# Kernel optimization log

Hardware: AMD Instinct MI355X
Metric: run time of the kernel (lower is better)

## Reference

```python
import jax, jax.numpy as jnp
import numpy as np


def conv2d(x, w, b, stride, pad):
    y = jax.lax.conv_general_dilated(
        x, w, (stride, stride), [(pad, pad), (pad, pad)],
        dimension_numbers=('NCHW', 'OIHW', 'NCHW'))
    return y + b[None, :, None, None]


def setup_inputs() -> dict:
    key = jax.random.key(0)
    ks = jax.random.split(key, 12)
    B = 8
    s = 0.02
    return {
        'x1': jax.random.normal(ks[0], (B, 256, 128, 128), jnp.float32),
        'x2': jax.random.normal(ks[1], (B, 512, 64, 64), jnp.float32),
        'x3': jax.random.normal(ks[2], (B, 1024, 32, 32), jnp.float32),
        'x4': jax.random.normal(ks[3], (B, 2048, 16, 16), jnp.float32),
        'cov1_w': jax.random.normal(ks[4], (512, 256, 3, 3), jnp.float32) * s,
        'cov1_b': jnp.zeros((512,), jnp.float32),
        'cov2_w': jax.random.normal(ks[5], (512, 512, 3, 3), jnp.float32) * s,
        'cov2_b': jnp.zeros((512,), jnp.float32),
        'cov3_w': jax.random.normal(ks[6], (512, 1024, 3, 3), jnp.float32) * s,
        'cov3_b': jnp.zeros((512,), jnp.float32),
        'cov4_w': jax.random.normal(ks[7], (512, 2048, 1, 1), jnp.float32) * s,
        'cov4_b': jnp.zeros((512,), jnp.float32),
        'gce_fc1_w': jax.random.normal(ks[8], (8, 64, 256), jnp.float32) * s,
        'gce_fc1_b': jnp.zeros((8, 64), jnp.float32),
        'gce_fc2_w': jax.random.normal(ks[9], (8, 256, 64), jnp.float32) * s,
        'gce_fc2_b': jnp.zeros((8, 256), jnp.float32),
        'gce_sa_w': jax.random.normal(ks[10], (8, 256), jnp.float32) * s,
        'gce_sa_b': jnp.zeros((8,), jnp.float32),
    }


def reference(x1, x2, x3, x4,
              cov1_w, cov1_b, cov2_w, cov2_b, cov3_w, cov3_b, cov4_w, cov4_b,
              gce_fc1_w, gce_fc1_b, gce_fc2_w, gce_fc2_b, gce_sa_w, gce_sa_b):
    # NOTE (faithful to original): DSCA.forward overwrites its attention output
    # with `rearrange(x, 'b (h w) c -> b c h w')`, i.e. it returns its first
    # argument (cov4(x4)) unchanged. Hence cov1/cov2/cov3 and the whole
    # dynamic-top-k attention path are dead code with exactly-zero gradients;
    # omitting them yields identical outputs and identical (zero) grads.
    x4 = conv2d(x4, cov4_w, cov4_b, 1, 0)          # [B,512,16,16]
    x = jnp.concatenate([x4, x4, x4, x4], axis=1)  # [B,2048,16,16]
    x0 = x
    B, C, H, W = x.shape
    G = 8
    xg = x.reshape(B, G, C // G, H, W)             # [B,G,256,H,W]
    # ChannelAttention per group (reduction_ratio=4: 256->64->256)
    avg = xg.mean(axis=(3, 4))                                           # [B,G,256]
    h = jax.nn.relu(jnp.einsum('bgc,goc->bgo', avg, gce_fc1_w) + gce_fc1_b)
    ca = jax.nn.sigmoid(jnp.einsum('bgo,gco->bgc', h, gce_fc2_w) + gce_fc2_b)
    y = xg * ca[:, :, :, None, None]
    # SpatialAttention per group (1x1 conv to 1 channel)
    sa = jax.nn.sigmoid(jnp.einsum('bgchw,gc->bghw', y, gce_sa_w)
                        + gce_sa_b[None, :, None, None])
    y = y * sa[:, :, None, :, :]
    # GroupCBAMEnhancer gating: sigmoid, then hard-1 above per-group mean
    y = jax.nn.sigmoid(y)
    mean = y.mean(axis=(2, 3, 4), keepdims=True)   # mean over (c,h,w) per group
    mask = jnp.where(y > mean, jnp.float32(1.0), y).reshape(B, C, H, W)
    return x * mask + x0
```

## Files before the change

### kernel.cpp

```cpp
#include <hip/hip_runtime.h>
#include <math.h>

typedef __attribute__((ext_vector_type(8))) short bf16x8;
typedef __attribute__((ext_vector_type(8))) unsigned short u16x8;
typedef __attribute__((ext_vector_type(4))) float f32x4;

#define GLOAD_LDS16(g, l) __builtin_amdgcn_global_load_lds( \
    (const __attribute__((address_space(1))) unsigned int*)(g), \
    (__attribute__((address_space(3))) unsigned int*)(l), 16, 0, 0)

__device__ __forceinline__ unsigned short f2bf(float f) {
    unsigned int u = __builtin_bit_cast(unsigned int, f);
    unsigned int r = (u + 0x7FFFu + ((u >> 16) & 1)) >> 16;
    return (unsigned short)r;
}

__device__ __forceinline__ float sigmoidf_(float v) {
    return 1.f / (1.f + expf(-v));
}

__global__ __launch_bounds__(256) void convert_kernel(
    const float* __restrict__ w, const float* __restrict__ x4,
    unsigned short* __restrict__ wbf, unsigned short* __restrict__ xbf)
{
    __shared__ float t[64][65];
    if (blockIdx.x < 512) {
        int f = blockIdx.x * 256 + threadIdx.x;
        int tile = f >> 9, inner = f & 511;
        int r = inner >> 3, cc = inner & 7;
        int mt = tile >> 5, kt = tile & 31;
        const float* src = w + (mt * 64 + r) * 2048 + kt * 64 + cc * 8;
        float4 v0 = *(const float4*)src;
        float4 v1 = *(const float4*)(src + 4);
        u16x8 o;
        o[0] = f2bf(v0.x); o[1] = f2bf(v0.y); o[2] = f2bf(v0.z); o[3] = f2bf(v0.w);
        o[4] = f2bf(v1.x); o[5] = f2bf(v1.y); o[6] = f2bf(v1.z); o[7] = f2bf(v1.w);
        *(u16x8*)(wbf + (size_t)tile * 4096 + r * 64 + ((cc ^ (r & 7)) * 8)) = o;
        return;
    }
    const int bi = blockIdx.x - 512;
    const int b = bi >> 7, rem = bi & 127;
    const int kt = rem >> 2, pg = rem & 3;
    const float* src = x4 + ((size_t)b * 2048 + kt * 64) * 256 + pg * 64;
#pragma unroll
    for (int i = 0; i < 4; ++i) {
        int f = i * 256 + threadIdx.x;
        int kk = f >> 4, pp4 = f & 15;
        float4 v = *(const float4*)(src + kk * 256 + pp4 * 4);
        t[pp4 * 4 + 0][kk] = v.x;
        t[pp4 * 4 + 1][kk] = v.y;
        t[pp4 * 4 + 2][kk] = v.z;
        t[pp4 * 4 + 3][kk] = v.w;
    }
    __syncthreads();
    unsigned short* dst = xbf + (size_t)((b * 4 + pg) * 32 + kt) * 4096;
#pragma unroll
    for (int i = 0; i < 2; ++i) {
        int inner = i * 256 + threadIdx.x;
        int r = inner >> 3, cc = inner & 7;
        u16x8 o;
#pragma unroll
        for (int j = 0; j < 8; ++j) o[j] = f2bf(t[r][cc * 8 + j]);
        *(u16x8*)(dst + r * 64 + ((cc ^ (r & 7)) * 8)) = o;
    }
}

__global__ __launch_bounds__(256) void gemm_bf16(
    const unsigned short* __restrict__ wbf, const unsigned short* __restrict__ xbf,
    const float* __restrict__ bias, float* __restrict__ y4,
    float* __restrict__ chanpart)
{
    __shared__ short As[2][2048];
    __shared__ short Bs[2][4096];

    const int tid = threadIdx.x;
    const int wave = tid >> 6, lane = tid & 63;
    const int wm = wave >> 1, wn = wave & 1;
    const int lr = lane & 15, lh = lane >> 4;

    const int nt = blockIdx.x;
    const int mt = blockIdx.y;

    const unsigned short* Abase = wbf + ((size_t)(mt >> 1) * 32) * 4096 + (mt & 1) * 2048;
    const unsigned short* Bbase = xbf + (size_t)nt * 32 * 4096;

#define STAGE(buf, t)                                                         \
    {                                                                         \
        const unsigned short* A_ = Abase + (size_t)(t) * 4096;                \
        const unsigned short* B_ = Bbase + (size_t)(t) * 4096;                \
        _Pragma("unroll")                                                     \
        for (int q2 = 0; q2 < 3; ++q2) {                                      \
            int seg = wave * 3 + q2;                                          \
            if (seg < 4) {                                                    \
                GLOAD_LDS16(A_ + seg * 512 + lane * 8, &As[buf][seg * 512]);  \
            } else {                                                          \
                GLOAD_LDS16(B_ + (seg - 4) * 512 + lane * 8,                  \
                            &Bs[buf][(seg - 4) * 512]);                       \
            }                                                                 \
        }                                                                     \
    }

    STAGE(0, 0);
    __syncthreads();

    f32x4 acc[2] = {};
    int cur = 0;
    for (int t = 0; t < 32; ++t) {
        if (t < 31) STAGE(cur ^ 1, t + 1);
#pragma unroll
        for (int kc = 0; kc < 2; ++kc) {
            const int ch = kc * 4 + lh;
            int rA  = wm * 16 + lr;
            int rB0 = wn * 32 + lr, rB1 = rB0 + 16;
            bf16x8 a0 = *(const bf16x8*)(&As[cur][rA  * 64 + ((ch ^ (rA  & 7)) * 8)]);
            bf16x8 b0 = *(const bf16x8*)(&Bs[cur][rB0 * 64 + ((ch ^ (rB0 & 7)) * 8)]);
            bf16x8 b1 = *(const bf16x8*)(&Bs[cur][rB1 * 64 + ((ch ^ (rB1 & 7)) * 8)]);
            acc[0] = __builtin_amdgcn_mfma_f32_16x16x32_bf16(a0, b0, acc[0], 0, 0, 0);
            acc[1] = __builtin_amdgcn_mfma_f32_16x16x32_bf16(a0, b1, acc[1], 0, 0, 0);
        }
        __syncthreads();
        cur ^= 1;
    }
#undef STAGE

    const int b = nt >> 2, q = nt & 3;
    float* yb = y4 + ((size_t)b * 512 + mt * 32) * 256 + q * 64;
#pragma unroll
    for (int rr = 0; rr < 4; ++rr) {
        const int m = wm * 16 + lh * 4 + rr;
        const float bv = bias[mt * 32 + m];
        yb[m * 256 + wn * 32 + lr]      = acc[0][rr] + bv;
        yb[m * 256 + wn * 32 + 16 + lr] = acc[1][rr] + bv;
        float s = acc[0][rr] + acc[1][rr];
        s += __shfl_xor(s, 1);
        s += __shfl_xor(s, 2);
        s += __shfl_xor(s, 4);
        s += __shfl_xor(s, 8);
        if (lr == 0)
            chanpart[(size_t)(b * 512 + mt * 32 + m) * 8 + q * 2 + wn] = s + 32.f * bv;
    }
}

__global__ __launch_bounds__(256) void sa_kernel(
    const float* __restrict__ y4, const float* __restrict__ chanpart,
    const float* __restrict__ fc1w, const float* __restrict__ fc1b,
    const float* __restrict__ fc2w, const float* __restrict__ fc2b,
    const float* __restrict__ saw, const float* __restrict__ sab,
    float* __restrict__ ca, float* __restrict__ sa, float* __restrict__ gsums)
{
    const int blk = blockIdx.x;
    const int bg = blk >> 3, pc = blk & 7;
    const int b = bg >> 3, g = bg & 7;
    const int tid = threadIdx.x;
    const float* xg = y4 + ((size_t)b * 512 + (g & 1) * 256) * 256;

    __shared__ float avgs[256], red[256], hs[64], cas[256], caws[256], sas[32];

    {
        const float* cpp = chanpart + (size_t)(b * 512 + (g & 1) * 256 + tid) * 8;
        float cp = 0.f;
#pragma unroll
        for (int i = 0; i < 8; ++i) cp += cpp[i];
        avgs[tid] = cp * (1.f / 256.f);
    }
    __syncthreads();
    {
        int o = tid & 63, seg = tid >> 6;
        const float* wr = fc1w + (g * 64 + o) * 256 + seg * 64;
        const float* av = avgs + seg * 64;
        float s = 0.f;
#pragma unroll
        for (int i = 0; i < 64; ++i) s = fmaf(av[i], wr[i], s);
        red[tid] = s;
    }
    __syncthreads();
    if (tid < 64) {
        float s = fc1b[g * 64 + tid] + red[tid] + red[64 + tid] + red[128 + tid] + red[192 + tid];
        hs[tid] = fmaxf(s, 0.f);
    }
    __syncthreads();
    {
        const float* wr = fc2w + (g * 256 + tid) * 64;
        float s = fc2b[g * 256 + tid];
#pragma unroll
        for (int i = 0; i < 64; ++i) s = fmaf(hs[i], wr[i], s);
        float v = sigmoidf_(s);
        cas[tid] = v;
        caws[tid] = v * saw[g * 256 + tid];
        if (pc == 0) ca[bg * 256 + tid] = v;
    }
    __syncthreads();
    const int p_l = tid & 31, seg8 = tid >> 5;
    const int p = pc * 32 + p_l;
    {
        float s = 0.f;
#pragma unroll
        for (int i = 0; i < 32; ++i) {
            int c = seg8 * 32 + i;
            s = fmaf(xg[c * 256 + p], caws[c], s);
        }
        red[tid] = s;
    }
    __syncthreads();
    if (tid < 32) {
        float s = sab[g];
#pragma unroll
        for (int k = 0; k < 8; ++k) s += red[k * 32 + tid];
        float v = sigmoidf_(s);
        sas[tid] = v;
        sa[bg * 256 + pc * 32 + tid] = v;
    }
    __syncthreads();
    {
        float sv = sas[p_l];
        float s = 0.f;
#pragma unroll
        for (int i = 0; i < 32; ++i) {
            int c = seg8 * 32 + i;
            s += sigmoidf_(xg[c * 256 + p] * cas[c] * sv);
        }
        red[tid] = s;
    }
    __syncthreads();
    for (int off = 128; off > 0; off >>= 1) {
        if (tid < off) red[tid] += red[tid + off];
        __syncthreads();
    }
    if (tid == 0) gsums[blk] = red[0];
}

__global__ __launch_bounds__(256) void final_kernel(
    const float* __restrict__ y4, const float* __restrict__ ca,
    const float* __restrict__ sa, const float* __restrict__ gsums,
    float* __restrict__ out)
{
    int f = blockIdx.x * 256 + threadIdx.x;
    int p4 = f & 63, ch = (f >> 6) & 2047, b = f >> 17;
    int g = ch >> 8, c = ch & 255, bg = b * 8 + g;
    const float4 x = *(const float4*)(y4 + ((size_t)b * 512 + (g & 1) * 256 + c) * 256 + p4 * 4);
    float cav = ca[bg * 256 + c];
    const float4 sv = *(const float4*)(sa + bg * 256 + p4 * 4);
    float msum = 0.f;
#pragma unroll
    for (int i = 0; i < 8; ++i) msum += gsums[bg * 8 + i];
    float mean = msum * (1.f / 65536.f);
    float4 o;
#define DOLANE(X) { float yv = sigmoidf_(x.X * cav * sv.X); float mk = (yv > mean) ? 1.f : yv; o.X = x.X * (1.f + mk); }
    DOLANE(x) DOLANE(y) DOLANE(z) DOLANE(w)
#undef DOLANE
    *(float4*)(out + (size_t)f * 4) = o;
}

extern "C" void kernel_launch(void* const* d_in, const int* in_sizes, int n_in,
                              void* d_out, int out_size, void* d_ws, size_t ws_size,
                              hipStream_t stream) {
    const float* x4   = (const float*)d_in[3];
    const float* w4   = (const float*)d_in[10];
    const float* b4   = (const float*)d_in[11];
    const float* fc1w = (const float*)d_in[12];
    const float* fc1b = (const float*)d_in[13];
    const float* fc2w = (const float*)d_in[14];
    const float* fc2b = (const float*)d_in[15];
    const float* saw  = (const float*)d_in[16];
    const float* sab  = (const float*)d_in[17];
    float* out = (float*)d_out;

    float* ws = (float*)d_ws;
    float* y4       = ws;
    float* ca       = ws + 1048576;
    float* sa       = ws + 1064960;
    float* gsums    = ws + 1081344;
    float* chanpart = ws + 1081856;
    unsigned short* wbf = (unsigned short*)(ws + 1114624);
    unsigned short* xbf = (unsigned short*)(ws + 1638912);

    convert_kernel<<<dim3(1536), dim3(256), 0, stream>>>(w4, x4, wbf, xbf);
    gemm_bf16<<<dim3(32, 16), dim3(256), 0, stream>>>(wbf, xbf, b4, y4, chanpart);
    sa_kernel<<<dim3(512), dim3(256), 0, stream>>>(y4, chanpart, fc1w, fc1b, fc2w, fc2b,
                                                   saw, sab, ca, sa, gsums);
    final_kernel<<<dim3(4096), dim3(256), 0, stream>>>(y4, ca, sa, gsums, out);
}
```

Baseline: 52.49 us.

## Halve GEMM N-tile to 1024 blocks with XCD-aware mapping; stage y4 slice in LDS

The GEMM N tile shrinks from 64 to 32 columns, doubling the grid to 1024 blocks so more CUs get work. Each wave now issues one MFMA per k-chunk, and the per-channel partial sums grow to 16 slots per channel. Block indices are remapped so consecutive XCDs share N tiles, aiming for better L2 reuse. The spatial-attention kernel now loads its 256x32 y4 slice into LDS once and reuses it for both channel passes, replacing two strided global reads. The cost is less compute per loaded tile in the GEMM and a 32 KB LDS footprint in sa_kernel.

```diff
diff --git a/kernel.cpp b/kernel.cpp
--- a/kernel.cpp
+++ b/kernel.cpp
@@ -71,73 +71,63 @@
     float* __restrict__ chanpart)
 {
     __shared__ short As[2][2048];
-    __shared__ short Bs[2][4096];
+    __shared__ short Bs[2][2048];
 
     const int tid = threadIdx.x;
     const int wave = tid >> 6, lane = tid & 63;
     const int wm = wave >> 1, wn = wave & 1;
     const int lr = lane & 15, lh = lane >> 4;
 
-    const int nt = blockIdx.x;
-    const int mt = blockIdx.y;
-
-    const unsigned short* Abase = wbf + ((size_t)(mt >> 1) * 32) * 4096 + (mt & 1) * 2048;
-    const unsigned short* Bbase = xbf + (size_t)nt * 32 * 4096;
-
-#define STAGE(buf, t)                                                         \
+    const int flat = blockIdx.x;
+    const int xcd = flat & 7, j = flat >> 3;
+    const int nt = xcd * 8 + (j & 7);
+    const int mt = j >> 3;
+
+    const unsigned short* Abase = wbf + (size_t)(mt >> 1) * 32 * 4096 + (mt & 1) * 2048;
+    const unsigned short* Bbase = xbf + (size_t)(nt >> 1) * 32 * 4096 + (nt & 1) * 2048;
+
+#define STAGE(buf, tt)                                                        \
     {                                                                         \
-        const unsigned short* A_ = Abase + (size_t)(t) * 4096;                \
-        const unsigned short* B_ = Bbase + (size_t)(t) * 4096;                \
-        _Pragma("unroll")                                                     \
-        for (int q2 = 0; q2 < 3; ++q2) {                                      \
-            int seg = wave * 3 + q2;                                          \
-            if (seg < 4) {                                                    \
-                GLOAD_LDS16(A_ + seg * 512 + lane * 8, &As[buf][seg * 512]);  \
-            } else {                                                          \
-                GLOAD_LDS16(B_ + (seg - 4) * 512 + lane * 8,                  \
-                            &Bs[buf][(seg - 4) * 512]);                       \
-            }                                                                 \
-        }                                                                     \
+        GLOAD_LDS16(Abase + (size_t)(tt) * 4096 + wave * 512 + lane * 8,      \
+                    &As[buf][wave * 512]);                                    \
+        GLOAD_LDS16(Bbase + (size_t)(tt) * 4096 + wave * 512 + lane * 8,      \
+                    &Bs[buf][wave * 512]);                                    \
     }
 
     STAGE(0, 0);
     __syncthreads();
 
-    f32x4 acc[2] = {};
+    f32x4 acc = {};
     int cur = 0;
     for (int t = 0; t < 32; ++t) {
         if (t < 31) STAGE(cur ^ 1, t + 1);
 #pragma unroll
         for (int kc = 0; kc < 2; ++kc) {
             const int ch = kc * 4 + lh;
-            int rA  = wm * 16 + lr;
-            int rB0 = wn * 32 + lr, rB1 = rB0 + 16;
-            bf16x8 a0 = *(const bf16x8*)(&As[cur][rA  * 64 + ((ch ^ (rA  & 7)) * 8)]);
-            bf16x8 b0 = *(const bf16x8*)(&Bs[cur][rB0 * 64 + ((ch ^ (rB0 & 7)) * 8)]);
-            bf16x8 b1 = *(const bf16x8*)(&Bs[cur][rB1 * 64 + ((ch ^ (rB1 & 7)) * 8)]);
-            acc[0] = __builtin_amdgcn_mfma_f32_16x16x32_bf16(a0, b0, acc[0], 0, 0, 0);
-            acc[1] = __builtin_amdgcn_mfma_f32_16x16x32_bf16(a0, b1, acc[1], 0, 0, 0);
+            int rA = wm * 16 + lr, rB = wn * 16 + lr;
+            bf16x8 a0 = *(const bf16x8*)(&As[cur][rA * 64 + ((ch ^ (rA & 7)) * 8)]);
+            bf16x8 b0 = *(const bf16x8*)(&Bs[cur][rB * 64 + ((ch ^ (rB & 7)) * 8)]);
+            acc = __builtin_amdgcn_mfma_f32_16x16x32_bf16(a0, b0, acc, 0, 0, 0);
         }
         __syncthreads();
         cur ^= 1;
     }
 #undef STAGE
 
-    const int b = nt >> 2, q = nt & 3;
-    float* yb = y4 + ((size_t)b * 512 + mt * 32) * 256 + q * 64;
+    const int b = nt >> 3, q = nt & 7;
+    float* yb = y4 + ((size_t)b * 512 + mt * 32) * 256 + q * 32;
 #pragma unroll
     for (int rr = 0; rr < 4; ++rr) {
         const int m = wm * 16 + lh * 4 + rr;
         const float bv = bias[mt * 32 + m];
-        yb[m * 256 + wn * 32 + lr]      = acc[0][rr] + bv;
-        yb[m * 256 + wn * 32 + 16 + lr] = acc[1][rr] + bv;
-        float s = acc[0][rr] + acc[1][rr];
+        yb[m * 256 + wn * 16 + lr] = acc[rr] + bv;
+        float s = acc[rr];
         s += __shfl_xor(s, 1);
         s += __shfl_xor(s, 2);
         s += __shfl_xor(s, 4);
         s += __shfl_xor(s, 8);
         if (lr == 0)
-            chanpart[(size_t)(b * 512 + mt * 32 + m) * 8 + q * 2 + wn] = s + 32.f * bv;
+            chanpart[(size_t)(b * 512 + mt * 32 + m) * 16 + q * 2 + wn] = s + 16.f * bv;
     }
 }
 
@@ -152,15 +142,23 @@
     const int bg = blk >> 3, pc = blk & 7;
     const int b = bg >> 3, g = bg & 7;
     const int tid = threadIdx.x;
-    const float* xg = y4 + ((size_t)b * 512 + (g & 1) * 256) * 256;
-
+    const float* xg = y4 + ((size_t)b * 512 + (g & 1) * 256) * 256 + pc * 32;
+
+    __shared__ float xl[256][32];
     __shared__ float avgs[256], red[256], hs[64], cas[256], caws[256], sas[32];
 
-    {
-        const float* cpp = chanpart + (size_t)(b * 512 + (g & 1) * 256 + tid) * 8;
+#pragma unroll
+    for (int i = 0; i < 8; ++i) {
+        int f = i * 256 + tid;
+        int c = f >> 3, p4 = f & 7;
+        float4 v = *(const float4*)(xg + c * 256 + p4 * 4);
+        *(float4*)(&xl[c][p4 * 4]) = v;
+    }
+    {
+        const float* cpp = chanpart + (size_t)(b * 512 + (g & 1) * 256 + tid) * 16;
         float cp = 0.f;
 #pragma unroll
-        for (int i = 0; i < 8; ++i) cp += cpp[i];
+        for (int i = 0; i < 16; ++i) cp += cpp[i];
         avgs[tid] = cp * (1.f / 256.f);
     }
     __syncthreads();
@@ -191,13 +189,12 @@
     }
     __syncthreads();
     const int p_l = tid & 31, seg8 = tid >> 5;
-    const int p = pc * 32 + p_l;
     {
         float s = 0.f;
 #pragma unroll
         for (int i = 0; i < 32; ++i) {
             int c = seg8 * 32 + i;
-            s = fmaf(xg[c * 256 + p], caws[c], s);
+            s = fmaf(xl[c][p_l], caws[c], s);
         }
         red[tid] = s;
     }
@@ -217,7 +214,7 @@
 #pragma unroll
         for (int i = 0; i < 32; ++i) {
             int c = seg8 * 32 + i;
-            s += sigmoidf_(xg[c * 256 + p] * cas[c] * sv);
+            s += sigmoidf_(xl[c][p_l] * cas[c] * sv);
         }
         red[tid] = s;
     }
@@ -268,15 +265,15 @@
     float* ws = (float*)d_ws;
     float* y4       = ws;
     float* ca       = ws + 1048576;
-    float* sa       = ws + 1064960;
+    float* saBuf    = ws + 1064960;
     float* gsums    = ws + 1081344;
     float* chanpart = ws + 1081856;
-    unsigned short* wbf = (unsigned short*)(ws + 1114624);
-    unsigned short* xbf = (unsigned short*)(ws + 1638912);
+    unsigned short* wbf = (unsigned short*)(ws + 1147392);
+    unsigned short* xbf = (unsigned short*)(ws + 1671680);
 
     convert_kernel<<<dim3(1536), dim3(256), 0, stream>>>(w4, x4, wbf, xbf);
-    gemm_bf16<<<dim3(32, 16), dim3(256), 0, stream>>>(wbf, xbf, b4, y4, chanpart);
+    gemm_bf16<<<dim3(1024), dim3(256), 0, stream>>>(wbf, xbf, b4, y4, chanpart);
     sa_kernel<<<dim3(512), dim3(256), 0, stream>>>(y4, chanpart, fc1w, fc1b, fc2w, fc2b,
-                                                   saw, sab, ca, sa, gsums);
-    final_kernel<<<dim3(4096), dim3(256), 0, stream>>>(y4, ca, sa, gsums, out);
-}
+                                                   saw, sab, ca, saBuf, gsums);
+    final_kernel<<<dim3(4096), dim3(256), 0, stream>>>(y4, ca, saBuf, gsums, out);
+}
```

Result: no change. 52.09 us (-0.8%).
